# Kernel optimization log

Measured on AMD Instinct MI355X. Metric: run time of the kernel, lower is better.

Reference implementation:

```python
import jax, jax.numpy as jnp
import numpy as np

B, S, DIM, HEADS, FFN = 2, 2048, 2048, 16, 8192
HD = DIM // HEADS            # 128
F_, H_, W_ = 8, 16, 16       # F*H*W == S (video token grid)
CTX = 512
EPS = 1e-6


def _rope_tables(max_len=1024):
    # Wan-style rope_params: per-axis inverse-frequency tables, concatenated columns [22|21|21].
    c = HD // 2  # 64 complex channels
    splits = [c - 2 * (c // 3), c // 3, c // 3]
    pos = np.arange(max_len)[:, None].astype(np.float64)
    parts = []
    for d in splits:
        inv = 1.0 / (10000.0 ** (np.arange(d, dtype=np.float64) / d))
        parts.append(pos * inv[None, :])
    theta = np.concatenate(parts, axis=1)  # [max_len, 64]
    return (jnp.asarray(np.cos(theta), jnp.float32),
            jnp.asarray(np.sin(theta), jnp.float32))


def setup_inputs() -> dict:
    key = jax.random.key(0)
    ks = iter(jax.random.split(key, 40))
    def nrm(shape, scale=1.0):
        return jax.random.normal(next(ks), shape, jnp.float32) * scale
    ws = DIM ** -0.5
    cos, sin = _rope_tables()
    inp = dict(
        x=nrm((B, S, DIM)),
        e=nrm((B, 6, DIM)),
        context=nrm((B, CTX, DIM)),
        freqs_cos=cos, freqs_sin=sin,
        modulation=nrm((1, 6, DIM), ws),
        # self-attention (weights stored [in, out] so y = x @ W + b)
        sa_wq=nrm((DIM, DIM), ws), sa_bq=jnp.zeros((DIM,), jnp.float32),
        sa_wk=nrm((DIM, DIM), ws), sa_bk=jnp.zeros((DIM,), jnp.float32),
        sa_wv=nrm((DIM, DIM), ws), sa_bv=jnp.zeros((DIM,), jnp.float32),
        sa_wo=nrm((DIM, DIM), ws), sa_bo=jnp.zeros((DIM,), jnp.float32),
        sa_nq=jnp.ones((DIM,), jnp.float32), sa_nk=jnp.ones((DIM,), jnp.float32),
        # t2v cross-attention
        ca_wq=nrm((DIM, DIM), ws), ca_bq=jnp.zeros((DIM,), jnp.float32),
        ca_wk=nrm((DIM, DIM), ws), ca_bk=jnp.zeros((DIM,), jnp.float32),
        ca_wv=nrm((DIM, DIM), ws), ca_bv=jnp.zeros((DIM,), jnp.float32),
        ca_wo=nrm((DIM, DIM), ws), ca_bo=jnp.zeros((DIM,), jnp.float32),
        ca_nq=jnp.ones((DIM,), jnp.float32), ca_nk=jnp.ones((DIM,), jnp.float32),
        norm3_w=jnp.ones((DIM,), jnp.float32), norm3_b=jnp.zeros((DIM,), jnp.float32),
        ffn_w1=nrm((DIM, FFN), ws), ffn_b1=jnp.zeros((FFN,), jnp.float32),
        ffn_w2=nrm((FFN, DIM), FFN ** -0.5), ffn_b2=jnp.zeros((DIM,), jnp.float32),
    )
    return inp


def _ln(x, w=None, b=None, eps=EPS):
    m = jnp.mean(x, -1, keepdims=True)
    v = jnp.mean((x - m) ** 2, -1, keepdims=True)
    y = (x - m) * jax.lax.rsqrt(v + eps)
    return y * w + b if w is not None else y


def _rms(x, w, eps=EPS):
    return x * jax.lax.rsqrt(jnp.mean(x * x, -1, keepdims=True) + eps) * w


def _grid_cs(tab):
    # tab: [1024, 64] -> per-token table [S, 64] for grid (F_,H_,W_), split 22/21/21
    c = HD // 2
    s0 = c - 2 * (c // 3)  # 22
    s1 = c // 3            # 21
    f = jnp.broadcast_to(tab[:F_, :s0][:, None, None, :], (F_, H_, W_, s0))
    h = jnp.broadcast_to(tab[:H_, s0:s0 + s1][None, :, None, :], (F_, H_, W_, s1))
    w = jnp.broadcast_to(tab[:W_, s0 + s1:][None, None, :, :], (F_, H_, W_, s1))
    return jnp.concatenate([f, h, w], -1).reshape(S, c)


def _rope(x, cos, sin):
    # x: [B,S,N,D]; complex rotation on consecutive (even, odd) pairs
    xp = x.reshape(*x.shape[:-1], HD // 2, 2)
    xr, xi = xp[..., 0], xp[..., 1]
    c = cos[None, :, None, :]
    s = sin[None, :, None, :]
    return jnp.stack([xr * c - xi * s, xr * s + xi * c], -1).reshape(x.shape)


def _attn(q, k, v):
    logits = jnp.einsum('bqnd,bknd->bnqk', q, k) / np.float32(np.sqrt(HD))
    w = jax.nn.softmax(logits, axis=-1)
    return jnp.einsum('bnqk,bknd->bqnd', w, v)


def reference(x, e, context, freqs_cos, freqs_sin, modulation,
              sa_wq, sa_bq, sa_wk, sa_bk, sa_wv, sa_bv, sa_wo, sa_bo, sa_nq, sa_nk,
              ca_wq, ca_bq, ca_wk, ca_bk, ca_wv, ca_bv, ca_wo, ca_bo, ca_nq, ca_nk,
              norm3_w, norm3_b, ffn_w1, ffn_b1, ffn_w2, ffn_b2,
              seq_lens=None, grid_sizes=None, context_lens=None):
    # AdaLN modulation: 6 (shift, scale, gate) vectors per sample
    em = modulation + e                       # [B,6,D]
    e0, e1, e2, e3, e4, e5 = [em[:, i:i + 1, :] for i in range(6)]
    cos = _grid_cs(freqs_cos)
    sin = _grid_cs(freqs_sin)

    # --- self-attention with modulated LayerNorm + 3D RoPE ---
    xn = _ln(x) * (1 + e1) + e0
    q = _rms(xn @ sa_wq + sa_bq, sa_nq).reshape(B, S, HEADS, HD)
    k = _rms(xn @ sa_wk + sa_bk, sa_nk).reshape(B, S, HEADS, HD)
    v = (xn @ sa_wv + sa_bv).reshape(B, S, HEADS, HD)
    y = _attn(_rope(q, cos, sin), _rope(k, cos, sin), v).reshape(B, S, DIM)
    x = x + (y @ sa_wo + sa_bo) * e2

    # --- t2v cross-attention (affine norm3) ---
    xn3 = _ln(x, norm3_w, norm3_b)
    q = _rms(xn3 @ ca_wq + ca_bq, ca_nq).reshape(B, S, HEADS, HD)
    k = _rms(context @ ca_wk + ca_bk, ca_nk).reshape(B, CTX, HEADS, HD)
    v = (context @ ca_wv + ca_bv).reshape(B, CTX, HEADS, HD)
    y = _attn(q, k, v).reshape(B, S, DIM)
    x = x + (y @ ca_wo + ca_bo)

    # --- modulated FFN (GELU-tanh) ---
    xn2 = _ln(x) * (1 + e4) + e3
    y = jax.nn.gelu(xn2 @ ffn_w1 + ffn_b1, approximate=True) @ ffn_w2 + ffn_b2
    return x + y * e5
```

## Files before the change

### kernel.cpp

```cpp
#include <hip/hip_runtime.h>
#include <hip/hip_bf16.h>
#include <math.h>

#define DIMX 2048
#define SLEN 2048
#define BSZ 2
#define NHEADS 16
#define HDIM 128
#define FFND 8192
#define CTXL 512
#define LN_EPS 1e-6f

typedef __attribute__((ext_vector_type(8))) short short8_t;
typedef __attribute__((ext_vector_type(4))) short short4_t;
typedef __attribute__((ext_vector_type(4))) float f32x4;
typedef __hip_bfloat16 bf16;

__device__ __forceinline__ short f2bf(float f) {
  union { float f; unsigned u; } v; v.f = f;
  return (short)((v.u + 0x7FFFu + ((v.u >> 16) & 1u)) >> 16);
}
__device__ __forceinline__ float bf2f(short s) {
  union { unsigned u; float f; } v; v.u = ((unsigned)(unsigned short)s) << 16;
  return v.f;
}

__device__ __forceinline__ void gload16(const void* g, void* l) {
  __builtin_amdgcn_global_load_lds(
      (const __attribute__((address_space(1))) unsigned int*)g,
      (__attribute__((address_space(3))) unsigned int*)l, 16, 0, 0);
}

__device__ __forceinline__ float wred_sum(float v) {
#pragma unroll
  for (int o = 32; o > 0; o >>= 1) v += __shfl_xor(v, o, 64);
  return v;
}

__global__ void em_kernel(const float* __restrict__ e, const float* __restrict__ mod,
                          float* __restrict__ em, int n) {
  int i = blockIdx.x * 256 + threadIdx.x;
  if (i < n) em[i] = e[i] + mod[i % (6 * DIMX)];
}

__global__ void cvt_kernel(const float* __restrict__ in, bf16* __restrict__ out, int n8) {
  int i = blockIdx.x * 256 + threadIdx.x;
  if (i >= n8) return;
  float4 a = *(const float4*)(in + (size_t)i * 8);
  float4 b = *(const float4*)(in + (size_t)i * 8 + 4);
  float fv[8] = {a.x, a.y, a.z, a.w, b.x, b.y, b.z, b.w};
  short8_t o;
#pragma unroll
  for (int j = 0; j < 8; ++j) o[j] = f2bf(fv[j]);
  *(short8_t*)((short*)out + (size_t)i * 8) = o;
}

__global__ void packb_kernel(const float* b0, const float* b1, const float* b2,
                             float* __restrict__ dst, int n) {
  int i = blockIdx.x * 256 + threadIdx.x;
  if (i >= n) return;
  int seg = i >> 11, j = i & 2047;
  const float* s = seg == 0 ? b0 : (seg == 1 ? b1 : b2);
  dst[i] = s[j];
}

__global__ __launch_bounds__(256) void combine_kernel(
    const bf16* __restrict__ p0, const bf16* __restrict__ p1,
    const float* __restrict__ bias, const float* __restrict__ resid,
    const float* __restrict__ scale, int scstride, int rows_per_b,
    float* __restrict__ out, int N) {
  int i8 = blockIdx.x * 256 + threadIdx.x;
  size_t base = (size_t)i8 * 8;
  int n = (int)(base % N);
  int m = (int)(base / N);
  int b = m / rows_per_b;
  short8_t a = *(const short8_t*)((const short*)p0 + base);
  short8_t c = *(const short8_t*)((const short*)p1 + base);
  const float* bi = bias + n;
  const float* sc = scale + (size_t)b * scstride + n;
  const float* rs = resid + base;
  float* o = out + base;
#pragma unroll
  for (int j = 0; j < 8; ++j)
    o[j] = rs[j] + (bf2f(a[j]) + bf2f(c[j]) + bi[j]) * sc[j];
}

__global__ __launch_bounds__(256) void transpose_w(const float* __restrict__ W,
                                                   bf16* __restrict__ Wt, int K, int N,
                                                   int noff) {
  __shared__ short tile[64 * 68];
  int k0 = blockIdx.y << 6, n0 = blockIdx.x << 6;
  int t = threadIdx.x;
#pragma unroll
  for (int p = 0; p < 4; ++p) {
    int lin = p * 1024 + t * 4;
    int kr = lin >> 6, nc = lin & 63;
    float4 f = *(const float4*)(W + (size_t)(k0 + kr) * N + n0 + nc);
    tile[(nc + 0) * 68 + kr] = f2bf(f.x);
    tile[(nc + 1) * 68 + kr] = f2bf(f.y);
    tile[(nc + 2) * 68 + kr] = f2bf(f.z);
    tile[(nc + 3) * 68 + kr] = f2bf(f.w);
  }
  __syncthreads();
#pragma unroll
  for (int p = 0; p < 4; ++p) {
    int lin = p * 1024 + t * 4;
    int nr = lin >> 6, kc = lin & 63;
    short4_t s = *(const short4_t*)&tile[nr * 68 + kc];
    *(short4_t*)((short*)Wt + (size_t)(noff + n0 + nr) * K + k0 + kc) = s;
  }
}

__global__ __launch_bounds__(256) void ln_kernel(
    const float* __restrict__ x, const float* __restrict__ gamma,
    const float* __restrict__ beta, int gbstride, float addone,
    int rows_per_b, bf16* __restrict__ out) {
  int row = blockIdx.x;
  int t = threadIdx.x;
  const float* xr = x + (size_t)row * DIMX;
  float4 v0 = *(const float4*)(xr + t * 8);
  float4 v1 = *(const float4*)(xr + t * 8 + 4);
  float vv[8] = {v0.x, v0.y, v0.z, v0.w, v1.x, v1.y, v1.z, v1.w};
  float s = 0.f, ss = 0.f;
#pragma unroll
  for (int i = 0; i < 8; ++i) { s += vv[i]; ss += vv[i] * vv[i]; }
  __shared__ float red[8];
  s = wred_sum(s); ss = wred_sum(ss);
  int wid = t >> 6;
  if ((t & 63) == 0) { red[wid] = s; red[4 + wid] = ss; }
  __syncthreads();
  float sum = red[0] + red[1] + red[2] + red[3];
  float sumsq = red[4] + red[5] + red[6] + red[7];
  float mean = sum * (1.f / DIMX);
  float var = sumsq * (1.f / DIMX) - mean * mean;
  float rs = rsqrtf(var + LN_EPS);
  int b = row / rows_per_b;
  const float* g = gamma + (size_t)b * gbstride;
  const float* be = beta + (size_t)b * gbstride;
  short8_t o;
#pragma unroll
  for (int i = 0; i < 8; ++i) {
    int d = t * 8 + i;
    float y = (vv[i] - mean) * rs;
    o[i] = f2bf(y * (addone + g[d]) + be[d]);
  }
  *(short8_t*)((short*)out + (size_t)row * DIMX + t * 8) = o;
}

__global__ __launch_bounds__(256) void rms_rope_kernel(
    const bf16* __restrict__ x, int xstride, const float* __restrict__ w,
    const float* __restrict__ fcos, const float* __restrict__ fsin,
    int do_rope, bf16* __restrict__ out) {
  int row = blockIdx.x;
  int t = threadIdx.x;
  short8_t xi = *(const short8_t*)((const short*)x + (size_t)row * xstride + t * 8);
  float vv[8];
#pragma unroll
  for (int i = 0; i < 8; ++i) vv[i] = bf2f(xi[i]);
  float ss = 0.f;
#pragma unroll
  for (int i = 0; i < 8; ++i) ss += vv[i] * vv[i];
  __shared__ float red[4];
  ss = wred_sum(ss);
  int wid = t >> 6;
  if ((t & 63) == 0) red[wid] = ss;
  __syncthreads();
  float sumsq = red[0] + red[1] + red[2] + red[3];
  float rs = rsqrtf(sumsq * (1.f / DIMX) + LN_EPS);
  float y[8];
#pragma unroll
  for (int i = 0; i < 8; ++i) y[i] = vv[i] * rs * w[t * 8 + i];
  if (do_rope) {
    int s = row % SLEN;
    int f = s >> 8, hh = (s >> 4) & 15, ww = s & 15;
    int jb = ((t * 8) % HDIM) >> 1;
#pragma unroll
    for (int p = 0; p < 4; ++p) {
      int j = jb + p;
      int src = (j < 22) ? f : ((j < 43) ? hh : ww);
      float c = fcos[src * 64 + j];
      float sn = fsin[src * 64 + j];
      float xr_ = y[2 * p], xim = y[2 * p + 1];
      y[2 * p] = xr_ * c - xim * sn;
      y[2 * p + 1] = xr_ * sn + xim * c;
    }
  }
  short8_t o;
#pragma unroll
  for (int i = 0; i < 8; ++i) o[i] = f2bf(y[i]);
  *(short8_t*)((short*)out + (size_t)row * DIMX + t * 8) = o;
}

#define RDAe(dst, bufL, mh) { _Pragma("unroll") for (int mi = 0; mi < 4; ++mi) { \
    dst[mi][0] = *(const short8_t*)&AsF[aA[mi][0] + (mh) * 4096 + (bufL) * 16384]; \
    dst[mi][1] = *(const short8_t*)&AsF[aA[mi][1] + (mh) * 4096 + (bufL) * 16384]; } }
#define RDBe(dst, bufL, nh) { _Pragma("unroll") for (int nj = 0; nj < 2; ++nj) { \
    dst[nj][0] = *(const short8_t*)&BsF[aB[nj][0] + (nh) * 2048 + (bufL) * 16384]; \
    dst[nj][1] = *(const short8_t*)&BsF[aB[nj][1] + (nh) * 2048 + (bufL) * 16384]; } }
#define MMAQ(aS, bS, mh, nh) { _Pragma("unroll") for (int kq = 0; kq < 2; ++kq) \
    _Pragma("unroll") for (int mi = 0; mi < 4; ++mi) \
    _Pragma("unroll") for (int nj = 0; nj < 2; ++nj) \
      acc[(mh)*4+mi][(nh)*2+nj] = __builtin_amdgcn_mfma_f32_16x16x32_bf16( \
          aS[mi][kq], bS[nj][kq], acc[(mh)*4+mi][(nh)*2+nj], 0, 0, 0); }
#define STA(bufL, kkE, late) { _Pragma("unroll") for (int i = 0; i < 2; ++i) \
    gload16(Ap + gA[i][late] + (kkE), &AsF[ldsA[i][late] + (bufL) * 16384]); }
#define STB(bufL, kkE, late) { _Pragma("unroll") for (int i = 0; i < 2; ++i) \
    gload16(Bp + gB[i][late] + (kkE), &BsF[ldsB[i][late] + (bufL) * 16384]); }
#define BAR asm volatile("s_barrier" ::: "memory")
#define VMCNT(n) asm volatile("s_waitcnt vmcnt(" #n ")" ::: "memory")
#define SETPRIO(x) __builtin_amdgcn_s_setprio(x)

__global__ __launch_bounds__(512) void gemm256(
    const bf16* __restrict__ A, const bf16* __restrict__ Bt,
    const float* __restrict__ bias,
    float* outF, bf16* outB,
    const float* resid, const float* __restrict__ scale,
    int scstride, int rows_per_b, int gn, int N, int K,
    int klen, int nsplit, long long spoff, int mode) {
  __shared__ short AsF[2 * 16384];
  __shared__ short BsF[2 * 16384];
  int t = threadIdx.x, lane = t & 63, wv = t >> 6;
  int l15 = lane & 15, koff = lane >> 4;
  int wm = wv >> 2, wn = wv & 3;
  int nwgx = gridDim.x, ksp = 0, bid = blockIdx.x;
  if (nsplit == 2) { nwgx >>= 1; if (bid >= nwgx) { ksp = 1; bid -= nwgx; } }
  int cpx = nwgx >> 3;
  int swz = (bid & 7) * cpx + (bid >> 3);
  int by = swz / gn, bx = swz % gn;
  int m0 = by << 8, n0 = bx << 8;
  int kbeg = ksp * klen;

  f32x4 acc[8][4] = {};
  short8_t ae[4][2], al[4][2], be[2][2], bl[2][2];

  int aA[4][2], aB[2][2];
#pragma unroll
  for (int mi = 0; mi < 4; ++mi) {
    int r = wm * 128 + mi * 16 + l15;
#pragma unroll
    for (int kq = 0; kq < 2; ++kq)
      aA[mi][kq] = r * 64 + (((kq * 4 + koff) ^ (r & 7)) << 3);
  }
#pragma unroll
  for (int nj = 0; nj < 2; ++nj) {
    int r = wn * 64 + nj * 16 + l15;
#pragma unroll
    for (int kq = 0; kq < 2; ++kq)
      aB[nj][kq] = r * 64 + (((kq * 4 + koff) ^ (r & 7)) << 3);
  }

  int srcChunk = ((lane & 7) ^ (lane >> 3)) << 3;
  int rowInSlot = lane >> 3;
  const short* Ap = (const short*)A;
  const short* Bp = (const short*)Bt;
  size_t gA[2][2], gB[2][2];
  int ldsA[2][2], ldsB[2][2];
#pragma unroll
  for (int i = 0; i < 2; ++i) {
    int idx = i * 8 + wv;
#pragma unroll
    for (int late = 0; late < 2; ++late) {
      int slotA = ((idx >> 3) << 4) + (idx & 7) + late * 8;
      gA[i][late] = (size_t)(m0 + slotA * 8 + rowInSlot) * K + srcChunk;
      ldsA[i][late] = slotA << 9;
      int slotB = ((idx >> 2) << 3) + (idx & 3) + late * 4;
      gB[i][late] = (size_t)(n0 + slotB * 8 + rowInSlot) * K + srcChunk;
      ldsB[i][late] = slotB << 9;
    }
  }

  int NT = klen >> 6;
  STA(0, kbeg, 0); STB(0, kbeg, 0); STA(0, kbeg, 1); STB(0, kbeg, 1);
  STA(1, kbeg + 64, 0); STB(1, kbeg + 64, 0);
  VMCNT(4); BAR;

  for (int tt = 0; tt < NT; tt += 2) {
    int k1 = kbeg + (((tt + 1) < NT ? (tt + 1) : 0) << 6);
    int k2 = kbeg + (((tt + 2) < NT ? (tt + 2) : 0) << 6);
    int k3 = kbeg + (((tt + 3) < NT ? (tt + 3) : 0) << 6);
    RDAe(ae, 0, 0); RDBe(be, 0, 0);
    STA(1, k1, 1);
    BAR; SETPRIO(1); MMAQ(ae, be, 0, 0); SETPRIO(0); RDBe(bl, 0, 1); BAR;
    STB(1, k1, 1);
    BAR; SETPRIO(1); MMAQ(ae, bl, 0, 1); SETPRIO(0); RDAe(al, 0, 1); BAR;
    STA(0, k2, 0);
    BAR; SETPRIO(1); MMAQ(al, bl, 1, 1); SETPRIO(0); BAR;
    STB(0, k2, 0);
    BAR; SETPRIO(1); MMAQ(al, be, 1, 0); SETPRIO(0); VMCNT(4); BAR;
    RDAe(ae, 1, 0); RDBe(be, 1, 0);
    STA(0, k2, 1);
    BAR; SETPRIO(1); MMAQ(ae, be, 0, 0); SETPRIO(0); RDBe(bl, 1, 1); BAR;
    STB(0, k2, 1);
    BAR; SETPRIO(1); MMAQ(ae, bl, 0, 1); SETPRIO(0); RDAe(al, 1, 1); BAR;
    STA(1, k3, 0);
    BAR; SETPRIO(1); MMAQ(al, bl, 1, 1); SETPRIO(0); BAR;
    STB(1, k3, 0);
    BAR; SETPRIO(1); MMAQ(al, be, 1, 0); SETPRIO(0); VMCNT(4); BAR;
  }
  VMCNT(0);

  int mo = m0 + wm * 128, no = n0 + wn * 64;
  long long so = (long long)ksp * spoff;
#pragma unroll
  for (int mf = 0; mf < 8; ++mf)
#pragma unroll
    for (int nf = 0; nf < 4; ++nf) {
      int n = no + nf * 16 + l15;
      float bia = (mode == 5) ? 0.f : bias[n];
#pragma unroll
      for (int r = 0; r < 4; ++r) {
        int m = mo + mf * 16 + koff * 4 + r;
        float vv = acc[mf][nf][r] + bia;
        size_t idx = (size_t)m * N + n;
        if (mode == 1) {
          ((short*)outB)[idx] = f2bf(vv);
        } else if (mode == 2) {
          float g = 0.5f * vv * (1.f + tanhf(0.7978845608f * (vv + 0.044715f * vv * vv * vv)));
          ((short*)outB)[idx] = f2bf(g);
        } else if (mode == 5) {
          ((short*)outB)[idx + so] = f2bf(vv);
        } else {
          float sc = scale ? scale[(size_t)(m / rows_per_b) * scstride + n] : 1.0f;
          outF[idx] = resid[idx] + vv * sc;
        }
      }
    }
}

__global__ __launch_bounds__(256) void gemm_bt(
    const bf16* __restrict__ A, const bf16* __restrict__ Bt,
    const float* __restrict__ bias,
    float* outF, bf16* outB,
    const float* resid, const float* __restrict__ scale,
    int scstride, int rows_per_b, int gn, int N, int K, int mode) {
  __shared__ short As[2][128 * 64];
  __shared__ short Bs[2][128 * 64];
  int t = threadIdx.x, lane = t & 63, wv = t >> 6;
  int nwg = gridDim.x, cpx = nwg >> 3;
  int swz = (blockIdx.x & 7) * cpx + (blockIdx.x >> 3);
  int by = swz / gn, bx = swz % gn;
  int m0 = by << 7, n0 = bx << 7;
  f32x4 acc[4][4] = {};
  int mo_l = (wv >> 1) << 6, no_l = (wv & 1) << 6;

  int srow[4], scol[4];
#pragma unroll
  for (int j = 0; j < 4; ++j) {
    srow[j] = wv * 32 + j * 8 + (lane >> 3);
    scol[j] = ((lane & 7) ^ (srow[j] & 7)) << 3;
  }
  const short* Ap = (const short*)A;
  const short* Bp = (const short*)Bt;

  int koff = lane >> 4;
  int rowA[4], rowB[4];
#pragma unroll
  for (int i = 0; i < 4; ++i) {
    rowA[i] = mo_l + i * 16 + (lane & 15);
    rowB[i] = no_l + i * 16 + (lane & 15);
  }

  auto stage = [&](int bufI, int kk) {
#pragma unroll
    for (int j = 0; j < 4; ++j) {
      gload16(Ap + (size_t)(m0 + srow[j]) * K + kk + scol[j],
              &As[bufI][(wv * 32 + j * 8) * 64]);
      gload16(Bp + (size_t)(n0 + srow[j]) * K + kk + scol[j],
              &Bs[bufI][(wv * 32 + j * 8) * 64]);
    }
  };

  stage(0, 0);
  __syncthreads();
  int cur = 0;
  for (int kk = 0; kk < K; kk += 64) {
    int nxt = cur ^ 1;
    if (kk + 64 < K) stage(nxt, kk + 64);
    short8_t af[2][4], bfv[2][4];
#pragma unroll
    for (int h = 0; h < 2; ++h)
#pragma unroll
      for (int i = 0; i < 4; ++i) {
        int cA = ((h * 4 + koff) ^ (rowA[i] & 7)) << 3;
        af[h][i] = *(const short8_t*)&As[cur][rowA[i] * 64 + cA];
        int cB = ((h * 4 + koff) ^ (rowB[i] & 7)) << 3;
        bfv[h][i] = *(const short8_t*)&Bs[cur][rowB[i] * 64 + cB];
      }
#pragma unroll
    for (int h = 0; h < 2; ++h)
#pragma unroll
      for (int mt = 0; mt < 4; ++mt)
#pragma unroll
        for (int nt = 0; nt < 4; ++nt)
          acc[mt][nt] = __builtin_amdgcn_mfma_f32_16x16x32_bf16(af[h][mt], bfv[h][nt], acc[mt][nt], 0, 0, 0);
    __syncthreads();
    cur = nxt;
  }

  int mo = m0 + mo_l, no = n0 + no_l;
#pragma unroll
  for (int mt = 0; mt < 4; ++mt)
#pragma unroll
    for (int nt = 0; nt < 4; ++nt) {
      int n = no + nt * 16 + (lane & 15);
      float bia = bias[n];
#pragma unroll
      for (int r = 0; r < 4; ++r) {
        int m = mo + mt * 16 + (lane >> 4) * 4 + r;
        float vv = acc[mt][nt][r] + bia;
        size_t idx = (size_t)m * N + n;
        if (mode == 1) {
          ((short*)outB)[idx] = f2bf(vv);
        } else if (mode == 2) {
          float g = 0.5f * vv * (1.f + tanhf(0.7978845608f * (vv + 0.044715f * vv * vv * vv)));
          ((short*)outB)[idx] = f2bf(g);
        } else {
          float sc = scale ? scale[(size_t)(m / rows_per_b) * scstride + n] : 1.0f;
          outF[idx] = resid[idx] + vv * sc;
        }
      }
    }
}

__global__ __launch_bounds__(512) void attn_kernel(
    const bf16* __restrict__ q, const bf16* __restrict__ k,
    const bf16* __restrict__ v, bf16* __restrict__ y,
    int QL, int KVL, int qs, int ks, int vs, float scl) {
  __shared__ short Kt[64 * 136];
  __shared__ short Vt[128 * 72];
  __shared__ unsigned Pl[128 * 36];
  __shared__ float rl[8 * 16];
  __shared__ float ll[8 * 16];
  int t = threadIdx.x, lane = t & 63, wv = t >> 6;
  int l15 = lane & 15, koff = lane >> 4;
  int bh = blockIdx.y;
  int b = bh / NHEADS, h = bh % NHEADS;
  int q0 = blockIdx.x * 128 + wv * 16;
  const short* qp = (const short*)q;
  const short* kp = (const short*)k;
  const short* vp = (const short*)v;
  const float c1 = scl * 1.44269504088896f;
  short8_t qf[4];
  {
    size_t qbase = ((size_t)(b * QL) + q0 + l15) * qs + h * HDIM + koff * 8;
#pragma unroll
    for (int kc = 0; kc < 4; ++kc) qf[kc] = *(const short8_t*)(qp + qbase + kc * 32);
  }
  f32x4 o[8] = {};
  float m_run = -1e30f, l_run = 0.f;
  int strow = t >> 3, stcol = (t & 7) * 16;
  for (int kt0 = 0; kt0 < KVL; kt0 += 64) {
    const short* ksrc = kp + ((size_t)(b * KVL + kt0 + strow) * ks + h * HDIM + stcol);
    const short* vsrc = vp + ((size_t)(b * KVL + kt0 + strow) * vs + h * HDIM + stcol);
#pragma unroll
    for (int c = 0; c < 2; ++c)
      *(short8_t*)&Kt[strow * 136 + stcol + c * 8] = *(const short8_t*)(ksrc + c * 8);
#pragma unroll
    for (int c = 0; c < 2; ++c) {
      short8_t vvv = *(const short8_t*)(vsrc + c * 8);
#pragma unroll
      for (int e = 0; e < 8; ++e) {
        int d = stcol + c * 8 + e;
        Vt[d * 72 + (strow ^ ((d >> 2) & 0x38))] = vvv[e];
      }
    }
    __syncthreads();
    f32x4 st[4];
#pragma unroll
    for (int kt = 0; kt < 4; ++kt) {
      f32x4 aa = {0.f, 0.f, 0.f, 0.f};
#pragma unroll
      for (int kc = 0; kc < 4; ++kc) {
        short8_t kf = *(const short8_t*)&Kt[(kt * 16 + l15) * 136 + kc * 32 + koff * 8];
        aa = __builtin_amdgcn_mfma_f32_16x16x32_bf16(kf, qf[kc], aa, 0, 0, 0);
      }
      st[kt] = aa;
    }
    float mt_ = -1e30f;
#pragma unroll
    for (int kt = 0; kt < 4; ++kt)
#pragma unroll
      for (int r = 0; r < 4; ++r) mt_ = fmaxf(mt_, st[kt][r]);
    mt_ = fmaxf(mt_, __shfl_xor(mt_, 16, 64));
    mt_ = fmaxf(mt_, __shfl_xor(mt_, 32, 64));
    float mtc = mt_ * c1;
    bool nos = __all(mtc <= m_run + 8.0f);
    float m_new = nos ? m_run : fmaxf(m_run, mtc);
    float ps = 0.f;
#pragma unroll
    for (int kt = 0; kt < 4; ++kt)
#pragma unroll
      for (int r = 0; r < 4; ++r) {
        float p = exp2f(fmaf(st[kt][r], c1, -m_new));
        st[kt][r] = p;
        ps += p;
      }
    ps += __shfl_xor(ps, 16, 64);
    ps += __shfl_xor(ps, 32, 64);
    if (!nos) {
      float rfac = exp2f(m_run - m_new);
      l_run = l_run * rfac + ps;
      m_run = m_new;
      if (lane < 16) rl[wv * 16 + lane] = rfac;
      float rr[4];
#pragma unroll
      for (int r = 0; r < 4; ++r) rr[r] = rl[wv * 16 + koff * 4 + r];
#pragma unroll
      for (int dt = 0; dt < 8; ++dt)
#pragma unroll
        for (int r = 0; r < 4; ++r) o[dt][r] *= rr[r];
    } else {
      l_run += ps;
    }
#pragma unroll
    for (int kt = 0; kt < 4; ++kt)
#pragma unroll
      for (int rp = 0; rp < 2; ++rp) {
        unsigned lo = (unsigned short)f2bf(st[kt][2 * rp]);
        unsigned hi = (unsigned short)f2bf(st[kt][2 * rp + 1]);
        Pl[(wv * 16 + l15) * 36 + kt * 8 + koff * 2 + rp] = lo | (hi << 16);
      }
#pragma unroll
    for (int kc2 = 0; kc2 < 2; ++kc2) {
      short8_t pa = *(const short8_t*)&Pl[(wv * 16 + l15) * 36 + kc2 * 16 + koff * 4];
#pragma unroll
      for (int dt = 0; dt < 8; ++dt) {
        int drow = dt * 16 + l15;
        int kv0 = (kc2 * 32 + koff * 8) ^ ((drow >> 2) & 0x38);
        short8_t vf = *(const short8_t*)&Vt[drow * 72 + kv0];
        o[dt] = __builtin_amdgcn_mfma_f32_16x16x32_bf16(pa, vf, o[dt], 0, 0, 0);
      }
    }
    __syncthreads();
  }
  if (lane < 16) ll[wv * 16 + lane] = 1.f / l_run;
  float li[4];
#pragma unroll
  for (int r = 0; r < 4; ++r) li[r] = ll[wv * 16 + koff * 4 + r];
  short* yp = (short*)y;
#pragma unroll
  for (int dt = 0; dt < 8; ++dt)
#pragma unroll
    for (int r = 0; r < 4; ++r) {
      int qq = q0 + koff * 4 + r;
      int d = dt * 16 + l15;
      yp[((size_t)(b * QL) + qq) * DIMX + h * HDIM + d] = f2bf(o[dt][r] * li[r]);
    }
}

#define OFF_EM    0ull
#define OFF_BQKV  (512ull << 10)
#define OFF_BCKV  (560ull << 10)
#define OFF_XN    (1ull << 20)
#define OFF_QKV   (17ull << 20)
#define OFF_CAQ   (17ull << 20)
#define OFF_KV    (33ull << 20)
#define OFF_QB    (65ull << 20)
#define OFF_KB    (81ull << 20)
#define OFF_YB    (97ull << 20)
#define OFF_CTX   (113ull << 20)
#define OFF_WBUF  (117ull << 20)
#define OFF_HB    (17ull << 20)
#define OFF_PS    (65ull << 20)

extern "C" void kernel_launch(void* const* d_in, const int* in_sizes, int n_in,
                              void* d_out, int out_size, void* d_ws, size_t ws_size,
                              hipStream_t stream) {
  const float* x       = (const float*)d_in[0];
  const float* e       = (const float*)d_in[1];
  const float* context = (const float*)d_in[2];
  const float* fcos    = (const float*)d_in[3];
  const float* fsin    = (const float*)d_in[4];
  const float* modu    = (const float*)d_in[5];
  const float* sa_wq = (const float*)d_in[6];  const float* sa_bq = (const float*)d_in[7];
  const float* sa_wk = (const float*)d_in[8];  const float* sa_bk = (const float*)d_in[9];
  const float* sa_wv = (const float*)d_in[10]; const float* sa_bv = (const float*)d_in[11];
  const float* sa_wo = (const float*)d_in[12]; const float* sa_bo = (const float*)d_in[13];
  const float* sa_nq = (const float*)d_in[14]; const float* sa_nk = (const float*)d_in[15];
  const float* ca_wq = (const float*)d_in[16]; const float* ca_bq = (const float*)d_in[17];
  const float* ca_wk = (const float*)d_in[18]; const float* ca_bk = (const float*)d_in[19];
  const float* ca_wv = (const float*)d_in[20]; const float* ca_bv = (const float*)d_in[21];
  const float* ca_wo = (const float*)d_in[22]; const float* ca_bo = (const float*)d_in[23];
  const float* ca_nq = (const float*)d_in[24]; const float* ca_nk = (const float*)d_in[25];
  const float* n3_w  = (const float*)d_in[26]; const float* n3_b  = (const float*)d_in[27];
  const float* f_w1  = (const float*)d_in[28]; const float* f_b1  = (const float*)d_in[29];
  const float* f_w2  = (const float*)d_in[30]; const float* f_b2  = (const float*)d_in[31];

  char* ws = (char*)d_ws;
  float* em   = (float*)(ws + OFF_EM);
  float* bqkv = (float*)(ws + OFF_BQKV);
  float* bckv = (float*)(ws + OFF_BCKV);
  bf16* xn    = (bf16*)(ws + OFF_XN);
  bf16* qkvb  = (bf16*)(ws + OFF_QKV);
  bf16* caqb  = (bf16*)(ws + OFF_CAQ);
  bf16* kvb   = (bf16*)(ws + OFF_KV);
  bf16* qb    = (bf16*)(ws + OFF_QB);
  bf16* kb    = (bf16*)(ws + OFF_KB);
  bf16* yb    = (bf16*)(ws + OFF_YB);
  bf16* ctxb  = (bf16*)(ws + OFF_CTX);
  bf16* wbuf  = (bf16*)(ws + OFF_WBUF);
  bf16* hb    = (bf16*)(ws + OFF_HB);
  bf16* ps    = (bf16*)(ws + OFF_PS);
  float* xw   = (float*)d_out;

  const int M = BSZ * SLEN;
  const int MC = BSZ * CTXL;
  const float scl = 0.08838834764831845f;

#define TRANSO(W, Kd, Nd, noff) \
  transpose_w<<<dim3((Nd) / 64, (Kd) / 64), 256, 0, stream>>>(W, wbuf, Kd, Nd, noff)
#define GEMM256(Am, Md, Nd, Kd, bias, oF, oB, res, sc, scs, rpb, mode) \
  gemm256<<<((Md) / 256) * ((Nd) / 256), 512, 0, stream>>>(Am, wbuf, bias, oF, oB, res, sc, \
                                                           scs, rpb, (Nd) / 256, Nd, Kd, Kd, 1, 0ll, mode)
#define GEMM128(Am, Md, Nd, Kd, bias, oF, oB, res, sc, scs, rpb, mode) \
  gemm_bt<<<((Md) / 128) * ((Nd) / 128), 256, 0, stream>>>(Am, wbuf, bias, oF, oB, res, sc, scs, rpb, (Nd) / 128, Nd, Kd, mode)

  em_kernel<<<(BSZ * 6 * DIMX + 255) / 256, 256, 0, stream>>>(e, modu, em, BSZ * 6 * DIMX);
  cvt_kernel<<<(MC * DIMX / 8 + 255) / 256, 256, 0, stream>>>(context, ctxb, MC * DIMX / 8);
  packb_kernel<<<(3 * DIMX + 255) / 256, 256, 0, stream>>>(sa_bq, sa_bk, sa_bv, bqkv, 3 * DIMX);
  packb_kernel<<<(2 * DIMX + 255) / 256, 256, 0, stream>>>(ca_bk, ca_bv, nullptr, bckv, 2 * DIMX);

  ln_kernel<<<M, 256, 0, stream>>>(x, em + 1 * DIMX, em + 0 * DIMX, 6 * DIMX, 1.0f, SLEN, xn);

  TRANSO(sa_wq, DIMX, DIMX, 0);
  TRANSO(sa_wk, DIMX, DIMX, DIMX);
  TRANSO(sa_wv, DIMX, DIMX, 2 * DIMX);
  GEMM256(xn, M, 3 * DIMX, DIMX, bqkv, nullptr, qkvb, nullptr, nullptr, 0, 1, 1);
  rms_rope_kernel<<<M, 256, 0, stream>>>(qkvb, 3 * DIMX, sa_nq, fcos, fsin, 1, qb);
  rms_rope_kernel<<<M, 256, 0, stream>>>((bf16*)((short*)qkvb + DIMX), 3 * DIMX, sa_nk, fcos, fsin, 1, kb);

  attn_kernel<<<dim3(SLEN / 128, BSZ * NHEADS), 512, 0, stream>>>(
      qb, kb, (bf16*)((short*)qkvb + 2 * DIMX), yb, SLEN, SLEN, DIMX, DIMX, 3 * DIMX, scl);

  TRANSO(sa_wo, DIMX, DIMX, 0);
  GEMM128(yb, M, DIMX, DIMX, sa_bo, xw, nullptr, x, em + 2 * DIMX, 6 * DIMX, SLEN, 3);

  ln_kernel<<<M, 256, 0, stream>>>(xw, n3_w, n3_b, 0, 0.0f, SLEN, xn);

  TRANSO(ca_wq, DIMX, DIMX, 0);
  GEMM128(xn, M, DIMX, DIMX, ca_bq, nullptr, caqb, nullptr, nullptr, 0, 1, 1);
  rms_rope_kernel<<<M, 256, 0, stream>>>(caqb, DIMX, ca_nq, fcos, fsin, 0, qb);

  TRANSO(ca_wk, DIMX, DIMX, 0);
  TRANSO(ca_wv, DIMX, DIMX, DIMX);
  GEMM128(ctxb, MC, 2 * DIMX, DIMX, bckv, nullptr, kvb, nullptr, nullptr, 0, 1, 1);
  rms_rope_kernel<<<MC, 256, 0, stream>>>(kvb, 2 * DIMX, ca_nk, fcos, fsin, 0, kb);

  attn_kernel<<<dim3(SLEN / 128, BSZ * NHEADS), 512, 0, stream>>>(
      qb, kb, (bf16*)((short*)kvb + DIMX), yb, SLEN, CTXL, DIMX, DIMX, 2 * DIMX, scl);

  TRANSO(ca_wo, DIMX, DIMX, 0);
  GEMM128(yb, M, DIMX, DIMX, ca_bo, xw, nullptr, xw, nullptr, 0, SLEN, 3);

  ln_kernel<<<M, 256, 0, stream>>>(xw, em + 4 * DIMX, em + 3 * DIMX, 6 * DIMX, 1.0f, SLEN, xn);

  TRANSO(f_w1, DIMX, FFND, 0);
  GEMM256(xn, M, FFND, DIMX, f_b1, nullptr, hb, nullptr, nullptr, 0, 1, 2);

  TRANSO(f_w2, FFND, DIMX, 0);
  gemm256<<<2 * (M / 256) * (DIMX / 256), 512, 0, stream>>>(
      hb, wbuf, f_b2, nullptr, ps, nullptr, nullptr, 0, 1, DIMX / 256, DIMX,
      FFND, FFND / 2, 2, (long long)M * DIMX, 5);
  combine_kernel<<<M * DIMX / 8 / 256, 256, 0, stream>>>(
      ps, ps + (size_t)M * DIMX, f_b2, xw, em + 5 * DIMX, 6 * DIMX, SLEN, xw, DIMX);
}
```

Measured before the change: 1.032 ms.

## Switch 256x256 GEMM to 32x32x16 MFMA tiles and exp2-based GELU

Rewrites the main 256-tile GEMM inner product to use 32x32x16 bf16 MFMA instructions instead of 16x16x32. This changes the LDS fragment addressing, the accumulator layout and the epilogue row mapping. The larger MFMA shape halves the instruction count and cuts LDS reads per FLOP. The GELU epilogue also replaces tanhf with the equivalent sigmoid form computed through exp2f, which is cheaper. The cost is higher register pressure from 16-wide accumulators and possible LDS bank conflicts under the new access pattern.

```diff
diff --git a/kernel.cpp b/kernel.cpp
--- a/kernel.cpp
+++ b/kernel.cpp
@@ -14,6 +14,7 @@
 typedef __attribute__((ext_vector_type(8))) short short8_t;
 typedef __attribute__((ext_vector_type(4))) short short4_t;
 typedef __attribute__((ext_vector_type(4))) float f32x4;
+typedef __attribute__((ext_vector_type(16))) float f32x16;
 typedef __hip_bfloat16 bf16;
 
 __device__ __forceinline__ short f2bf(float f) {
@@ -191,17 +192,15 @@
   *(short8_t*)((short*)out + (size_t)row * DIMX + t * 8) = o;
 }
 
-#define RDAe(dst, bufL, mh) { _Pragma("unroll") for (int mi = 0; mi < 4; ++mi) { \
-    dst[mi][0] = *(const short8_t*)&AsF[aA[mi][0] + (mh) * 4096 + (bufL) * 16384]; \
-    dst[mi][1] = *(const short8_t*)&AsF[aA[mi][1] + (mh) * 4096 + (bufL) * 16384]; } }
-#define RDBe(dst, bufL, nh) { _Pragma("unroll") for (int nj = 0; nj < 2; ++nj) { \
-    dst[nj][0] = *(const short8_t*)&BsF[aB[nj][0] + (nh) * 2048 + (bufL) * 16384]; \
-    dst[nj][1] = *(const short8_t*)&BsF[aB[nj][1] + (nh) * 2048 + (bufL) * 16384]; } }
-#define MMAQ(aS, bS, mh, nh) { _Pragma("unroll") for (int kq = 0; kq < 2; ++kq) \
-    _Pragma("unroll") for (int mi = 0; mi < 4; ++mi) \
-    _Pragma("unroll") for (int nj = 0; nj < 2; ++nj) \
-      acc[(mh)*4+mi][(nh)*2+nj] = __builtin_amdgcn_mfma_f32_16x16x32_bf16( \
-          aS[mi][kq], bS[nj][kq], acc[(mh)*4+mi][(nh)*2+nj], 0, 0, 0); }
+#define RDA32(dst, bufL, mh) { _Pragma("unroll") for (int mi = 0; mi < 2; ++mi) \
+    _Pragma("unroll") for (int kq = 0; kq < 4; ++kq) \
+      dst[mi][kq] = *(const short8_t*)&AsF[aA[mi][kq] + (mh) * 4096 + (bufL) * 16384]; }
+#define RDB32(dst, bufL, nh) { _Pragma("unroll") for (int kq = 0; kq < 4; ++kq) \
+      dst[kq] = *(const short8_t*)&BsF[aB[kq] + (nh) * 2048 + (bufL) * 16384]; }
+#define MMAQ32(aS, bS, mh, nh) { _Pragma("unroll") for (int kq = 0; kq < 4; ++kq) \
+    _Pragma("unroll") for (int mi = 0; mi < 2; ++mi) \
+      acc[(mh)*2+mi][nh] = __builtin_amdgcn_mfma_f32_32x32x16_bf16( \
+          aS[mi][kq], bS[kq], acc[(mh)*2+mi][nh], 0, 0, 0); }
 #define STA(bufL, kkE, late) { _Pragma("unroll") for (int i = 0; i < 2; ++i) \
     gload16(Ap + gA[i][late] + (kkE), &AsF[ldsA[i][late] + (bufL) * 16384]); }
 #define STB(bufL, kkE, late) { _Pragma("unroll") for (int i = 0; i < 2; ++i) \
@@ -220,7 +219,7 @@
   __shared__ short AsF[2 * 16384];
   __shared__ short BsF[2 * 16384];
   int t = threadIdx.x, lane = t & 63, wv = t >> 6;
-  int l15 = lane & 15, koff = lane >> 4;
+  int l31 = lane & 31, l5 = lane >> 5;
   int wm = wv >> 2, wn = wv & 3;
   int nwgx = gridDim.x, ksp = 0, bid = blockIdx.x;
   if (nsplit == 2) { nwgx >>= 1; if (bid >= nwgx) { ksp = 1; bid -= nwgx; } }
@@ -230,23 +229,23 @@
   int m0 = by << 8, n0 = bx << 8;
   int kbeg = ksp * klen;
 
-  f32x4 acc[8][4] = {};
-  short8_t ae[4][2], al[4][2], be[2][2], bl[2][2];
-
-  int aA[4][2], aB[2][2];
-#pragma unroll
-  for (int mi = 0; mi < 4; ++mi) {
-    int r = wm * 128 + mi * 16 + l15;
-#pragma unroll
-    for (int kq = 0; kq < 2; ++kq)
-      aA[mi][kq] = r * 64 + (((kq * 4 + koff) ^ (r & 7)) << 3);
-  }
-#pragma unroll
-  for (int nj = 0; nj < 2; ++nj) {
-    int r = wn * 64 + nj * 16 + l15;
-#pragma unroll
-    for (int kq = 0; kq < 2; ++kq)
-      aB[nj][kq] = r * 64 + (((kq * 4 + koff) ^ (r & 7)) << 3);
+  f32x16 acc[4][2] = {};
+  short8_t ae[2][4], al[2][4], be[4], bl[4];
+
+  int aA[2][4], aB[4];
+#pragma unroll
+  for (int mi = 0; mi < 2; ++mi)
+#pragma unroll
+    for (int kq = 0; kq < 4; ++kq) {
+      int r = wm * 128 + mi * 32 + l31;
+      int c = kq * 2 + l5;
+      aA[mi][kq] = r * 64 + ((c ^ (r & 7)) << 3);
+    }
+#pragma unroll
+  for (int kq = 0; kq < 4; ++kq) {
+    int r = wn * 64 + l31;
+    int c = kq * 2 + l5;
+    aB[kq] = r * 64 + ((c ^ (r & 7)) << 3);
   }
 
   int srcChunk = ((lane & 7) ^ (lane >> 3)) << 3;
@@ -278,44 +277,45 @@
     int k1 = kbeg + (((tt + 1) < NT ? (tt + 1) : 0) << 6);
     int k2 = kbeg + (((tt + 2) < NT ? (tt + 2) : 0) << 6);
     int k3 = kbeg + (((tt + 3) < NT ? (tt + 3) : 0) << 6);
-    RDAe(ae, 0, 0); RDBe(be, 0, 0);
+    RDA32(ae, 0, 0); RDB32(be, 0, 0);
     STA(1, k1, 1);
-    BAR; SETPRIO(1); MMAQ(ae, be, 0, 0); SETPRIO(0); RDBe(bl, 0, 1); BAR;
+    BAR; SETPRIO(1); MMAQ32(ae, be, 0, 0); SETPRIO(0); RDB32(bl, 0, 1); BAR;
     STB(1, k1, 1);
-    BAR; SETPRIO(1); MMAQ(ae, bl, 0, 1); SETPRIO(0); RDAe(al, 0, 1); BAR;
+    BAR; SETPRIO(1); MMAQ32(ae, bl, 0, 1); SETPRIO(0); RDA32(al, 0, 1); BAR;
     STA(0, k2, 0);
-    BAR; SETPRIO(1); MMAQ(al, bl, 1, 1); SETPRIO(0); BAR;
+    BAR; SETPRIO(1); MMAQ32(al, bl, 1, 1); SETPRIO(0); BAR;
     STB(0, k2, 0);
-    BAR; SETPRIO(1); MMAQ(al, be, 1, 0); SETPRIO(0); VMCNT(4); BAR;
-    RDAe(ae, 1, 0); RDBe(be, 1, 0);
+    BAR; SETPRIO(1); MMAQ32(al, be, 1, 0); SETPRIO(0); VMCNT(4); BAR;
+    RDA32(ae, 1, 0); RDB32(be, 1, 0);
     STA(0, k2, 1);
-    BAR; SETPRIO(1); MMAQ(ae, be, 0, 0); SETPRIO(0); RDBe(bl, 1, 1); BAR;
+    BAR; SETPRIO(1); MMAQ32(ae, be, 0, 0); SETPRIO(0); RDB32(bl, 1, 1); BAR;
     STB(0, k2, 1);
-    BAR; SETPRIO(1); MMAQ(ae, bl, 0, 1); SETPRIO(0); RDAe(al, 1, 1); BAR;
+    BAR; SETPRIO(1); MMAQ32(ae, bl, 0, 1); SETPRIO(0); RDA32(al, 1, 1); BAR;
     STA(1, k3, 0);
-    BAR; SETPRIO(1); MMAQ(al, bl, 1, 1); SETPRIO(0); BAR;
+    BAR; SETPRIO(1); MMAQ32(al, bl, 1, 1); SETPRIO(0); BAR;
     STB(1, k3, 0);
-    BAR; SETPRIO(1); MMAQ(al, be, 1, 0); SETPRIO(0); VMCNT(4); BAR;
+    BAR; SETPRIO(1); MMAQ32(al, be, 1, 0); SETPRIO(0); VMCNT(4); BAR;
   }
   VMCNT(0);
 
   int mo = m0 + wm * 128, no = n0 + wn * 64;
   long long so = (long long)ksp * spoff;
 #pragma unroll
-  for (int mf = 0; mf < 8; ++mf)
-#pragma unroll
-    for (int nf = 0; nf < 4; ++nf) {
-      int n = no + nf * 16 + l15;
+  for (int mt = 0; mt < 4; ++mt)
+#pragma unroll
+    for (int nt = 0; nt < 2; ++nt) {
+      int n = no + nt * 32 + l31;
       float bia = (mode == 5) ? 0.f : bias[n];
 #pragma unroll
-      for (int r = 0; r < 4; ++r) {
-        int m = mo + mf * 16 + koff * 4 + r;
-        float vv = acc[mf][nf][r] + bia;
+      for (int r = 0; r < 16; ++r) {
+        int m = mo + mt * 32 + (r & 3) + 8 * (r >> 2) + 4 * l5;
+        float vv = acc[mt][nt][r] + bia;
         size_t idx = (size_t)m * N + n;
         if (mode == 1) {
           ((short*)outB)[idx] = f2bf(vv);
         } else if (mode == 2) {
-          float g = 0.5f * vv * (1.f + tanhf(0.7978845608f * (vv + 0.044715f * vv * vv * vv)));
+          float u = 0.7978845608f * (vv + 0.044715f * vv * vv * vv);
+          float g = vv / (1.f + exp2f(-2.88539009f * u));
           ((short*)outB)[idx] = f2bf(g);
         } else if (mode == 5) {
           ((short*)outB)[idx + so] = f2bf(vv);
```

Measured after the change: 1.052 ms. About the same (+2.0%).
